# Performance work log

Measured on AMD Instinct MI355X. Metric: run time of the kernel, lower is better.

The kernel has to match this reference:

```python
import jax, jax.numpy as jnp
import numpy as np
import math

N = 100000
E = 1600000
IN_DIM = 64
OUT_DIM = 64
EPS = 1e-5


def setup_inputs() -> dict:
    key = jax.random.key(0)
    ks = jax.random.split(key, 12)
    s = 1.0 / math.sqrt(IN_DIM)
    inp = {
        "geo_x": jax.random.normal(ks[0], (N, IN_DIM), dtype=jnp.float32),
        "euc_x": jax.random.normal(ks[1], (N, IN_DIM), dtype=jnp.float32),
        "Wq": jax.random.uniform(ks[2], (OUT_DIM, IN_DIM), minval=-s, maxval=s, dtype=jnp.float32),
        "bq": jnp.zeros((OUT_DIM,), jnp.float32),
        "Wk": jax.random.uniform(ks[3], (OUT_DIM, IN_DIM), minval=-s, maxval=s, dtype=jnp.float32),
        "bk": jnp.zeros((OUT_DIM,), jnp.float32),
        "Wv": jax.random.uniform(ks[4], (OUT_DIM, IN_DIM), minval=-s, maxval=s, dtype=jnp.float32),
        "bv": jnp.zeros((OUT_DIM,), jnp.float32),
        "Wskip": jax.random.uniform(ks[5], (OUT_DIM, IN_DIM), minval=-s, maxval=s, dtype=jnp.float32),
        "bskip": jnp.zeros((OUT_DIM,), jnp.float32),
        "ln_w": jnp.ones((OUT_DIM,), jnp.float32),
        "ln_b": jnp.zeros((OUT_DIM,), jnp.float32),
        "edge_index": jax.random.randint(ks[6], (2, E), 0, N, dtype=jnp.int64),
    }
    return inp


def reference(geo_x, euc_x, Wq, bq, Wk, bk, Wv, bv, Wskip, bskip, ln_w, ln_b, edge_index):
    n = euc_x.shape[0]
    src, dst = edge_index[0], edge_index[1]

    # TransformerConv, heads=1: q from target (euc), k/v from source (geo)
    q = euc_x @ Wq.T + bq                      # [N, C]
    k = geo_x @ Wk.T + bk                      # [N, C]
    v = geo_x @ Wv.T + bv                      # [N, C]
    C = q.shape[-1]

    # per-edge attention logits
    alpha = jnp.sum(q[dst] * k[src], axis=-1) / math.sqrt(C)   # [E]

    # segment softmax over incoming edges of each destination node
    amax = jax.ops.segment_max(alpha, dst, num_segments=n)
    amax = jnp.where(jnp.isfinite(amax), amax, 0.0)
    ex = jnp.exp(alpha - amax[dst])
    denom = jax.ops.segment_sum(ex, dst, num_segments=n)
    w = ex / (denom[dst] + 1e-16)                              # [E]

    # scatter-aggregate weighted values + root (skip) transform
    agg = jax.ops.segment_sum(w[:, None] * v[src], dst, num_segments=n)  # [N, C]
    out = agg + euc_x @ Wskip.T + bskip

    # PyG LayerNorm, mode='graph', batch=None: normalize over all nodes+channels
    mean = out.mean()
    xc = out - mean
    std = jnp.sqrt(jnp.mean(xc * xc))
    out = xc / (std + EPS) * ln_w + ln_b

    return jax.nn.relu(out)
```

## Files before the change

kernel.cpp:

```cpp
#include <hip/hip_runtime.h>
#include <hip/hip_fp16.h>


using short8 = __attribute__((ext_vector_type(8))) short;
using f32x4  = __attribute__((ext_vector_type(4))) float;
using h2     = __attribute__((ext_vector_type(2))) _Float16;

#define QSCALE 31.75f
#define VDESC  0.031496062992f
#define SCI    1.7889250e-4f

#define CAP   4608
#define NCBMAX 400

__device__ inline unsigned short f2bf(float f) {
    unsigned u = __float_as_uint(f);
    unsigned r = u + 0x7FFFu + ((u >> 16) & 1u);
    return (unsigned short)(r >> 16);
}
__device__ inline unsigned short f2h(float f) {
    union { _Float16 h; unsigned short u; } c;
    c.h = (_Float16)f;
    return c.u;
}
__device__ inline h2 u2h2(unsigned u) {
    union { unsigned u; h2 h; } c; c.u = u; return c.h;
}
__device__ inline signed char f2i8(float f) {
    float v = f * QSCALE;
    v = fminf(fmaxf(v, -127.f), 127.f);
    return (signed char)__float2int_rn(v);
}

__device__ inline float fexp2(float x) {
#if __has_builtin(__builtin_amdgcn_exp2f)
    return __builtin_amdgcn_exp2f(x);
#else
    return __expf(x * 0.6931471805599453f);
#endif
}

__device__ inline int dot8i(uint2 q, uint2 k) {
#if __has_builtin(__builtin_amdgcn_sdot4)
    int t = __builtin_amdgcn_sdot4((int)q.x, (int)k.x, 0, false);
    return  __builtin_amdgcn_sdot4((int)q.y, (int)k.y, t, false);
#else
    int t = 0;
    #pragma unroll
    for (int i = 0; i < 4; ++i) {
        int qa = (int)(q.x << (24 - 8 * i)) >> 24;
        int ka = (int)(k.x << (24 - 8 * i)) >> 24;
        int qb = (int)(q.y << (24 - 8 * i)) >> 24;
        int kb = (int)(k.y << (24 - 8 * i)) >> 24;
        t += qa * ka + qb * kb;
    }
    return t;
#endif
}

__global__ __launch_bounds__(256) void k0_wconv(
    const float* __restrict__ Wq, const float* __restrict__ Wk,
    const float* __restrict__ Wv, const float* __restrict__ Wsk,
    unsigned short* __restrict__ wbf, int* __restrict__ zbase, int zcount)
{
    if (blockIdx.x == 16) {
        for (int i = threadIdx.x; i < zcount; i += 256) zbase[i] = 0;
        return;
    }
    int mat = blockIdx.x >> 2;
    int i4  = (blockIdx.x & 3) * 256 + threadIdx.x;
    const float* W = (mat == 0) ? Wq : (mat == 1) ? Wk : (mat == 2) ? Wv : Wsk;
    float4 w = *(const float4*)(W + (long)i4 * 4);
    ushort4 o;
    o.x = f2bf(w.x); o.y = f2bf(w.y); o.z = f2bf(w.z); o.w = f2bf(w.w);
    *(ushort4*)(wbf + (long)mat * 4096 + (long)i4 * 4) = o;
}

__global__ __launch_bounds__(256, 3) void k1_proj(
    const float* __restrict__ geo, const float* __restrict__ euc,
    const unsigned short* __restrict__ wbf,
    const float* __restrict__ bq, const float* __restrict__ bk,
    const float* __restrict__ bv, const float* __restrict__ bsk,
    signed char* __restrict__ q8b, signed char* __restrict__ kv8,
    unsigned short* __restrict__ skb, int N)
{
    __shared__ __align__(16) char smem[4 * 64 * 208];
    const int tid  = threadIdx.x;
    const int lane = tid & 63;
    const int w    = tid >> 6;
    const int qq   = lane >> 4;
    const int m    = lane & 15;
    const long base = (long)blockIdx.x * 128;

    char* te0 = smem;
    char* te1 = smem + 64 * 208;
    char* tg0 = smem + 2 * 64 * 208;
    char* tg1 = smem + 3 * 64 * 208;

    const long nodeA0 = base + w * 16 + m;
    const long nodeA1 = base + 64 + w * 16 + m;

    auto loadA = [&](const float* __restrict__ x, long node, short8 a[2]) {
        const float* px = x + node * 64;
        const bool v = (node < N);
        #pragma unroll
        for (int kh = 0; kh < 2; ++kh) {
            float4 f0 = v ? *(const float4*)(px + kh * 32 + qq * 8)
                          : make_float4(0.f, 0.f, 0.f, 0.f);
            float4 f1 = v ? *(const float4*)(px + kh * 32 + qq * 8 + 4)
                          : make_float4(0.f, 0.f, 0.f, 0.f);
            short8 r;
            r[0] = (short)f2bf(f0.x); r[1] = (short)f2bf(f0.y);
            r[2] = (short)f2bf(f0.z); r[3] = (short)f2bf(f0.w);
            r[4] = (short)f2bf(f1.x); r[5] = (short)f2bf(f1.y);
            r[6] = (short)f2bf(f1.z); r[7] = (short)f2bf(f1.w);
            a[kh] = r;
        }
    };
    auto loadB = [&](int mat, short8 b[2][4]) {
        #pragma unroll
        for (int kh = 0; kh < 2; ++kh)
            #pragma unroll
            for (int nt = 0; nt < 4; ++nt)
                b[kh][nt] = *(const short8*)(wbf + (long)mat * 4096 +
                                             (nt * 16 + m) * 64 + kh * 32 + qq * 8);
    };
    auto mmul = [&](const short8 a[2], const short8 b[2][4], f32x4 acc[4]) {
        #pragma unroll
        for (int nt = 0; nt < 4; ++nt) acc[nt] = (f32x4)(0.f);
        #pragma unroll
        for (int kh = 0; kh < 2; ++kh)
            #pragma unroll
            for (int nt = 0; nt < 4; ++nt)
                acc[nt] = __builtin_amdgcn_mfma_f32_16x16x32_bf16(a[kh], b[kh][nt], acc[nt], 0, 0, 0);
    };

    auto emit_i8 = [&](const f32x4 acc[4], const float* __restrict__ bias, char* tile) {
        #pragma unroll
        for (int nt = 0; nt < 4; ++nt) {
            int c = nt * 16 + m;
            float bs = bias[c];
            #pragma unroll
            for (int r = 0; r < 4; ++r) {
                int nl = w * 16 + qq * 4 + r;
                *(signed char*)(tile + nl * 208 + c) = f2i8(acc[nt][r] + bs);
            }
        }
    };
    auto emit_h = [&](const f32x4 acc[4], const float* __restrict__ bias, char* tile) {
        #pragma unroll
        for (int nt = 0; nt < 4; ++nt) {
            int c = nt * 16 + m;
            float bs = bias[c];
            #pragma unroll
            for (int r = 0; r < 4; ++r) {
                int nl = w * 16 + qq * 4 + r;
                *(unsigned short*)(tile + nl * 208 + 64 + c * 2) = f2h(acc[nt][r] + bs);
            }
        }
    };
    auto emit_kv = [&](const f32x4 acc[4], const float* __restrict__ bias,
                       char* tile, int vpart) {
        #pragma unroll
        for (int nt = 0; nt < 4; ++nt) {
            int c = nt * 16 + m;
            float bs = bias[c];
            int boff = (c >> 3) * 16 + vpart * 8 + (c & 7);
            #pragma unroll
            for (int r = 0; r < 4; ++r) {
                int nl = w * 16 + qq * 4 + r;
                *(signed char*)(tile + nl * 208 + boff) = f2i8(acc[nt][r] + bs);
            }
        }
    };

    short8 a0[2], a1[2];
    short8 B0[2][4], B1[2][4];
    f32x4 acc[4];

    loadA(euc, nodeA0, a0);
    loadA(euc, nodeA1, a1);
    loadB(0, B0);
    loadB(3, B1);
    mmul(a0, B0, acc); emit_i8(acc, bq, te0);
    mmul(a1, B0, acc); emit_i8(acc, bq, te1);
    mmul(a0, B1, acc); emit_h(acc, bsk, te0);
    mmul(a1, B1, acc); emit_h(acc, bsk, te1);

    loadA(geo, nodeA0, a0);
    loadA(geo, nodeA1, a1);
    loadB(1, B0);
    loadB(2, B1);
    mmul(a0, B0, acc); emit_kv(acc, bk, tg0, 0);
    mmul(a1, B0, acc); emit_kv(acc, bk, tg1, 0);
    mmul(a0, B1, acc); emit_kv(acc, bv, tg0, 1);
    mmul(a1, B1, acc); emit_kv(acc, bv, tg1, 1);
    __syncthreads();

    #pragma unroll
    for (int t = 0; t < 2; ++t) {
        const char* te = t ? te1 : te0;
        const char* tg = t ? tg1 : tg0;
        const long tb = base + t * 64;
        {
            int n = tid >> 2, j = tid & 3;
            long nd = tb + n;
            if (nd < N)
                *(int4*)(q8b + nd * 64 + j * 16) = *(const int4*)(te + n * 208 + j * 16);
        }
        #pragma unroll
        for (int it = 0; it < 2; ++it) {
            int idx = it * 256 + tid;
            int n = idx >> 3, j = idx & 7;
            long nd = tb + n;
            if (nd < N)
                *(int4*)((char*)skb + nd * 128 + j * 16) =
                    *(const int4*)(te + n * 208 + 64 + j * 16);
        }
        #pragma unroll
        for (int it = 0; it < 2; ++it) {
            int idx = it * 256 + tid;
            int n = idx >> 3, j = idx & 7;
            long nd = tb + n;
            if (nd < N)
                *(int4*)(kv8 + nd * 128 + j * 16) = *(const int4*)(tg + n * 208 + j * 16);
        }
    }
}

__global__ __launch_bounds__(512) void k2a_part(
    const int* __restrict__ ei, int E, int N,
    int* __restrict__ ccur, unsigned* __restrict__ tmp)
{
    __shared__ unsigned ebuf[4096];
    __shared__ unsigned short cbuf[4096];
    __shared__ int h[NCBMAX], offA[NCBMAX], lc[NCBMAX], creg[NCBMAX];
    __shared__ int sc[512];

    const int tid = threadIdx.x;
    const int NCB = (N + 255) >> 8;
    const long e0 = (long)blockIdx.x * 4096;
    const int tileN = (int)(((long)E - e0 < 4096) ? ((long)E - e0) : 4096);

    for (int i = tid; i < NCB; i += 512) { h[i] = 0; lc[i] = 0; }
    __syncthreads();

    const int* srcp = ei;
    const int* dstp = ei + E;
    unsigned wj[8];
    int cbj[8];
    #pragma unroll
    for (int j = 0; j < 8; ++j) {
        int i = j * 512 + tid;
        wj[j] = 0u; cbj[j] = -1;
        if (i < tileN) {
            int d = dstp[e0 + i], s = srcp[e0 + i];
            cbj[j] = d >> 8;
            wj[j]  = ((unsigned)(d & 255) << 17) | (unsigned)s;
            atomicAdd(&h[cbj[j]], 1);
        }
    }
    __syncthreads();

    sc[tid] = (tid < NCB) ? h[tid] : 0;
    __syncthreads();
    int own = sc[tid];
    for (int off = 1; off < 512; off <<= 1) {
        int v = (tid >= off) ? sc[tid - off] : 0;
        __syncthreads();
        sc[tid] += v;
        __syncthreads();
    }
    if (tid < NCB) offA[tid] = sc[tid] - own;
    if (tid < NCB && h[tid] > 0)
        creg[tid] = atomicAdd(&ccur[tid], h[tid]);
    __syncthreads();

    #pragma unroll
    for (int j = 0; j < 8; ++j) {
        if (cbj[j] >= 0) {
            int pos = offA[cbj[j]] + atomicAdd(&lc[cbj[j]], 1);
            ebuf[pos] = wj[j];
            cbuf[pos] = (unsigned short)cbj[j];
        }
    }
    __syncthreads();

    #pragma unroll
    for (int j = 0; j < 8; ++j) {
        int i = j * 512 + tid;
        if (i < tileN) {
            int cb = cbuf[i];
            int r  = creg[cb] + (i - offA[cb]);
            if (r < CAP) tmp[(long)cb * CAP + r] = ebuf[i];
        }
    }
}

__global__ __launch_bounds__(512, 8) void k3_attn(
    const signed char* __restrict__ q8b, const signed char* __restrict__ kv8,
    const unsigned short* __restrict__ skb,
    const int* __restrict__ ccnt, const unsigned* __restrict__ tmp,
    float* __restrict__ out, float* __restrict__ partS, float* __restrict__ partSS,
    int N)
{
    __shared__ unsigned bkt[64 * 65];
    __shared__ int dcnt[64];
    __shared__ unsigned char perm[64];
    __shared__ float redS[8], redSS[8];
    const int tid  = threadIdx.x;
    const int lane = tid & 63;
    const int w    = tid >> 6;
    const int g0   = tid >> 3;
    const int gl   = tid & 7;
    const int bin  = blockIdx.x;
    const int cb   = bin >> 2;
    const unsigned sub = (unsigned)(bin & 3);
    const long nodeBase = (long)bin * 64;

    if (tid < 64) dcnt[tid] = 0;
    __syncthreads();

    int len = ccnt[cb];
    if (len > CAP) len = CAP;
    const unsigned* reg = tmp + (long)cb * CAP;
    for (int e = tid; e < len; e += 512) {
        unsigned wv = reg[e];
        if (((wv >> 23) & 3u) == sub) {
            int d = (wv >> 17) & 63;
            int slot = atomicAdd(&dcnt[d], 1);
            if (slot < 64) bkt[d * 65 + slot] = wv & 0x1FFFFu;
        }
    }
    __syncthreads();

    if (tid < 64) {
        int d = dcnt[tid]; if (d > 64) d = 64;
        int r = 0;
        for (int j = 0; j < 64; ++j) {
            int dj = dcnt[j]; if (dj > 64) dj = 64;
            r += (dj > d) || ((dj == d) && (j < tid));
        }
        perm[r] = (unsigned char)tid;
    }
    __syncthreads();

    const int row  = perm[g0];
    const long node = nodeBase + row;

    uint2 qu = make_uint2(0, 0);
    if (node < N) qu = *(const uint2*)(q8b + node * 64 + gl * 8);

    int deg = dcnt[row];
    if (deg > 64) deg = 64;

    float den = 0.f;
    float a0=0.f,a1=0.f,a2=0.f,a3=0.f,a4=0.f,a5=0.f,a6=0.f,a7=0.f;

    auto vacc = [&](unsigned vx, unsigned vy, float ex) {
        a0 = fmaf((float)((int)(vx << 24) >> 24), ex, a0);
        a1 = fmaf((float)((int)(vx << 16) >> 24), ex, a1);
        a2 = fmaf((float)((int)(vx <<  8) >> 24), ex, a2);
        a3 = fmaf((float)((int)(vx      ) >> 24), ex, a3);
        a4 = fmaf((float)((int)(vy << 24) >> 24), ex, a4);
        a5 = fmaf((float)((int)(vy << 16) >> 24), ex, a5);
        a6 = fmaf((float)((int)(vy <<  8) >> 24), ex, a6);
        a7 = fmaf((float)((int)(vy      ) >> 24), ex, a7);
    };

    if (deg > 0) {
        const int rb  = row * 65;
        const int dm1 = deg - 1;
        unsigned sA = bkt[rb];
        uint4 rA = *(const uint4*)(kv8 + (long)sA * 128 + gl * 16);

        for (int s = 0; s < deg; s += 2) {
            int i1 = (s + 1 < deg) ? s + 1 : dm1;
            unsigned sB = bkt[rb + i1];
            uint4 rB = *(const uint4*)(kv8 + (long)sB * 128 + gl * 16);

            int t0 = dot8i(qu, make_uint2(rA.x, rA.y));
            t0 += __shfl_xor(t0, 1);
            t0 += __shfl_xor(t0, 2);
            t0 += __shfl_xor(t0, 4);
            float ex0 = fexp2((float)t0 * SCI);
            den += ex0;
            vacc(rA.z, rA.w, ex0);

            int i2 = (s + 2 < deg) ? s + 2 : dm1;
            unsigned sC = bkt[rb + i2];
            rA = *(const uint4*)(kv8 + (long)sC * 128 + gl * 16);

            int t1 = dot8i(qu, make_uint2(rB.x, rB.y));
            t1 += __shfl_xor(t1, 1);
            t1 += __shfl_xor(t1, 2);
            t1 += __shfl_xor(t1, 4);
            float ex1 = (s + 1 < deg) ? fexp2((float)t1 * SCI) : 0.f;
            den += ex1;
            vacc(rB.z, rB.w, ex1);
        }
    }

    float sacc = 0.f, ssacc = 0.f;
    if (node < N) {
        float inv = VDESC / (den + 1e-16f);
        uint4 sk = *(const uint4*)((const char*)skb + node * 128 + gl * 16);
        h2 s0 = u2h2(sk.x), s1 = u2h2(sk.y), s2 = u2h2(sk.z), s3 = u2h2(sk.w);
        float o0 = a0 * inv + (float)s0.x, o1 = a1 * inv + (float)s0.y;
        float o2 = a2 * inv + (float)s1.x, o3 = a3 * inv + (float)s1.y;
        float o4 = a4 * inv + (float)s2.x, o5 = a5 * inv + (float)s2.y;
        float o6 = a6 * inv + (float)s3.x, o7 = a7 * inv + (float)s3.y;
        *(float4*)(out + node * 64 + gl * 8)     = make_float4(o0, o1, o2, o3);
        *(float4*)(out + node * 64 + gl * 8 + 4) = make_float4(o4, o5, o6, o7);
        sacc  = (o0 + o1 + o2 + o3) + (o4 + o5 + o6 + o7);
        ssacc = o0*o0 + o1*o1 + o2*o2 + o3*o3 + o4*o4 + o5*o5 + o6*o6 + o7*o7;
    }
    #pragma unroll
    for (int m = 1; m <= 32; m <<= 1) {
        sacc  += __shfl_xor(sacc, m);
        ssacc += __shfl_xor(ssacc, m);
    }
    if (lane == 0) { redS[w] = sacc; redSS[w] = ssacc; }
    __syncthreads();
    if (tid == 0) {
        float s = 0.f, ss = 0.f;
        #pragma unroll
        for (int i = 0; i < 8; ++i) { s += redS[i]; ss += redSS[i]; }
        partS[bin]  = s;
        partSS[bin] = ss;
    }
}

__global__ __launch_bounds__(256) void k35_stats(
    const float* __restrict__ partS, const float* __restrict__ partSS,
    int nparts, float* __restrict__ stats, float M)
{
    __shared__ float rs[256], rss[256];
    float s = 0.f, ss = 0.f;
    for (int i = threadIdx.x; i < nparts; i += 256) { s += partS[i]; ss += partSS[i]; }
    rs[threadIdx.x] = s; rss[threadIdx.x] = ss;
    __syncthreads();
    for (int st = 128; st > 0; st >>= 1) {
        if (threadIdx.x < st) {
            rs[threadIdx.x]  += rs[threadIdx.x + st];
            rss[threadIdx.x] += rss[threadIdx.x + st];
        }
        __syncthreads();
    }
    if (threadIdx.x == 0) {
        float mean = rs[0] / M;
        float var  = rss[0] / M - mean * mean;
        if (var < 0.f) var = 0.f;
        stats[0] = mean;
        stats[1] = 1.f / (sqrtf(var) + 1e-5f);
    }
}

__global__ __launch_bounds__(256) void k4_ln(
    float* __restrict__ out, const float* __restrict__ lnw,
    const float* __restrict__ lnb, const float* __restrict__ stats, int M4)
{
    int i = blockIdx.x * 256 + threadIdx.x;
    if (i >= M4) return;
    float mean = stats[0], scale = stats[1];
    float4 x = *(float4*)(out + (long)i * 4);
    int c4 = (i & 15) * 4;
    float4 wv = *(const float4*)(lnw + c4);
    float4 bv = *(const float4*)(lnb + c4);
    x.x = fmaxf((x.x - mean) * scale * wv.x + bv.x, 0.f);
    x.y = fmaxf((x.y - mean) * scale * wv.y + bv.y, 0.f);
    x.z = fmaxf((x.z - mean) * scale * wv.z + bv.z, 0.f);
    x.w = fmaxf((x.w - mean) * scale * wv.w + bv.w, 0.f);
    *(float4*)(out + (long)i * 4) = x;
}

extern "C" void kernel_launch(void* const* d_in, const int* in_sizes, int n_in,
                              void* d_out, int out_size, void* d_ws, size_t ws_size,
                              hipStream_t stream)
{
    const float* geo = (const float*)d_in[0];
    const float* euc = (const float*)d_in[1];
    const float* Wq  = (const float*)d_in[2];
    const float* bq  = (const float*)d_in[3];
    const float* Wk  = (const float*)d_in[4];
    const float* bk  = (const float*)d_in[5];
    const float* Wv  = (const float*)d_in[6];
    const float* bv  = (const float*)d_in[7];
    const float* Wsk = (const float*)d_in[8];
    const float* bsk = (const float*)d_in[9];
    const float* lnw = (const float*)d_in[10];
    const float* lnb = (const float*)d_in[11];
    const int*   ei  = (const int*)d_in[12];

    const int N = in_sizes[0] / 64;
    const int E = in_sizes[12] / 2;
    const int K = (N + 63) / 64;
    const int NCB = (N + 255) >> 8;
    float* out = (float*)d_out;

    char* p = (char*)d_ws;
    signed char*    q8b   = (signed char*)p;    p += (size_t)N * 64;
    signed char*    kv8   = (signed char*)p;    p += (size_t)N * 128;
    unsigned short* skb   = (unsigned short*)p; p += (size_t)N * 64 * 2;
    unsigned*       tmp   = (unsigned*)p;       p += (size_t)NCB * CAP * 4;
    unsigned short* wbf   = (unsigned short*)p; p += (size_t)4 * 4096 * 2;
    int* ccur = (int*)p;  p += (size_t)(NCB + 8) * 4;
    float* partS  = (float*)p; p += (size_t)K * 4;
    float* partSS = (float*)p; p += (size_t)K * 4;
    float* stats  = (float*)p;

    const int PB2 = (N + 127) / 128;

    k0_wconv<<<17, 256, 0, stream>>>(Wq, Wk, Wv, Wsk, wbf, ccur, NCB + 8);
    k1_proj<<<PB2, 256, 0, stream>>>(geo, euc, wbf, bq, bk, bv, bsk,
                                     q8b, kv8, skb, N);
    const int GA = (E + 4095) / 4096;
    k2a_part<<<GA, 512, 0, stream>>>(ei, E, N, ccur, tmp);
    k3_attn<<<K, 512, 0, stream>>>(q8b, kv8, skb, ccur, tmp, out, partS, partSS, N);
    k35_stats<<<1, 256, 0, stream>>>(partS, partSS, K, stats, (float)N * 64.0f);
    const int M4 = N * 16;
    k4_ln<<<(M4 + 255) / 256, 256, 0, stream>>>(out, lnw, lnb, stats, M4);
}
```

Before: 212.1 us.

## Store pre-norm output as fp16, widen attention bins, add nontemporal memory ops

The attention kernel now handles 128 destination nodes per block, two per 8-lane group, and stores the pre-LayerNorm result as packed fp16 in a new workspace buffer rather than fp32 in the output. The LayerNorm kernel reads that fp16 buffer and writes fp32 with nontemporal stores, cutting intermediate traffic. The projection kernel halves its shared memory by running the euc and geo phases one after the other, and its occupancy hint rises to 6. Streaming loads and stores across kernels use nontemporal builtins. The fp16 intermediate loses some precision, and the serialized projection phases add a barrier.

```diff
diff --git a/kernel.cpp b/kernel.cpp
--- a/kernel.cpp
+++ b/kernel.cpp
@@ -5,6 +5,9 @@
 using short8 = __attribute__((ext_vector_type(8))) short;
 using f32x4  = __attribute__((ext_vector_type(4))) float;
 using h2     = __attribute__((ext_vector_type(2))) _Float16;
+using u32x4  = __attribute__((ext_vector_type(4))) unsigned;
+using u32x2  = __attribute__((ext_vector_type(2))) unsigned;
+using f32x4v = __attribute__((ext_vector_type(4))) float;
 
 #define QSCALE 31.75f
 #define VDESC  0.031496062992f
@@ -12,6 +15,36 @@
 
 #define CAP   4608
 #define NCBMAX 400
+
+__device__ inline int ntload(const int* p) {
+    return __builtin_nontemporal_load(p);
+}
+__device__ inline unsigned ntload(const unsigned* p) {
+    return __builtin_nontemporal_load(p);
+}
+__device__ inline uint2 ntload(const uint2* p) {
+    u32x2 v = __builtin_nontemporal_load((const u32x2*)p);
+    return make_uint2(v.x, v.y);
+}
+__device__ inline uint4 ntload(const uint4* p) {
+    u32x4 v = __builtin_nontemporal_load((const u32x4*)p);
+    return make_uint4(v.x, v.y, v.z, v.w);
+}
+__device__ inline float4 ntload(const float4* p) {
+    f32x4v v = __builtin_nontemporal_load((const f32x4v*)p);
+    return make_float4(v.x, v.y, v.z, v.w);
+}
+__device__ inline void ntstore(unsigned* p, unsigned v) {
+    __builtin_nontemporal_store(v, p);
+}
+__device__ inline void ntstore(uint4* p, uint4 v) {
+    u32x4 t; t.x = v.x; t.y = v.y; t.z = v.z; t.w = v.w;
+    __builtin_nontemporal_store(t, (u32x4*)p);
+}
+__device__ inline void ntstore(float4* p, float4 v) {
+    f32x4v t; t.x = v.x; t.y = v.y; t.z = v.z; t.w = v.w;
+    __builtin_nontemporal_store(t, (f32x4v*)p);
+}
 
 __device__ inline unsigned short f2bf(float f) {
     unsigned u = __float_as_uint(f);
@@ -76,7 +109,7 @@
     *(ushort4*)(wbf + (long)mat * 4096 + (long)i4 * 4) = o;
 }
 
-__global__ __launch_bounds__(256, 3) void k1_proj(
+__global__ __launch_bounds__(256, 6) void k1_proj(
     const float* __restrict__ geo, const float* __restrict__ euc,
     const unsigned short* __restrict__ wbf,
     const float* __restrict__ bq, const float* __restrict__ bk,
@@ -84,7 +117,7 @@
     signed char* __restrict__ q8b, signed char* __restrict__ kv8,
     unsigned short* __restrict__ skb, int N)
 {
-    __shared__ __align__(16) char smem[4 * 64 * 208];
+    __shared__ __align__(16) char smem[2 * 64 * 208];
     const int tid  = threadIdx.x;
     const int lane = tid & 63;
     const int w    = tid >> 6;
@@ -92,10 +125,8 @@
     const int m    = lane & 15;
     const long base = (long)blockIdx.x * 128;
 
-    char* te0 = smem;
-    char* te1 = smem + 64 * 208;
-    char* tg0 = smem + 2 * 64 * 208;
-    char* tg1 = smem + 3 * 64 * 208;
+    char* t0 = smem;
+    char* t1 = smem + 64 * 208;
 
     const long nodeA0 = base + w * 16 + m;
     const long nodeA1 = base + 64 + w * 16 + m;
@@ -105,9 +136,9 @@
         const bool v = (node < N);
         #pragma unroll
         for (int kh = 0; kh < 2; ++kh) {
-            float4 f0 = v ? *(const float4*)(px + kh * 32 + qq * 8)
+            float4 f0 = v ? ntload((const float4*)(px + kh * 32 + qq * 8))
                           : make_float4(0.f, 0.f, 0.f, 0.f);
-            float4 f1 = v ? *(const float4*)(px + kh * 32 + qq * 8 + 4)
+            float4 f1 = v ? ntload((const float4*)(px + kh * 32 + qq * 8 + 4))
                           : make_float4(0.f, 0.f, 0.f, 0.f);
             short8 r;
             r[0] = (short)f2bf(f0.x); r[1] = (short)f2bf(f0.y);
@@ -182,25 +213,14 @@
     loadA(euc, nodeA1, a1);
     loadB(0, B0);
     loadB(3, B1);
-    mmul(a0, B0, acc); emit_i8(acc, bq, te0);
-    mmul(a1, B0, acc); emit_i8(acc, bq, te1);
-    mmul(a0, B1, acc); emit_h(acc, bsk, te0);
-    mmul(a1, B1, acc); emit_h(acc, bsk, te1);
-
-    loadA(geo, nodeA0, a0);
-    loadA(geo, nodeA1, a1);
-    loadB(1, B0);
-    loadB(2, B1);
-    mmul(a0, B0, acc); emit_kv(acc, bk, tg0, 0);
-    mmul(a1, B0, acc); emit_kv(acc, bk, tg1, 0);
-    mmul(a0, B1, acc); emit_kv(acc, bv, tg0, 1);
-    mmul(a1, B1, acc); emit_kv(acc, bv, tg1, 1);
-    __syncthreads();
-
+    mmul(a0, B0, acc); emit_i8(acc, bq, t0);
+    mmul(a1, B0, acc); emit_i8(acc, bq, t1);
+    mmul(a0, B1, acc); emit_h(acc, bsk, t0);
+    mmul(a1, B1, acc); emit_h(acc, bsk, t1);
+    __syncthreads();
     #pragma unroll
     for (int t = 0; t < 2; ++t) {
-        const char* te = t ? te1 : te0;
-        const char* tg = t ? tg1 : tg0;
+        const char* te = t ? t1 : t0;
         const long tb = base + t * 64;
         {
             int n = tid >> 2, j = tid & 3;
@@ -217,6 +237,22 @@
                 *(int4*)((char*)skb + nd * 128 + j * 16) =
                     *(const int4*)(te + n * 208 + 64 + j * 16);
         }
+    }
+    __syncthreads();
+
+    loadA(geo, nodeA0, a0);
+    loadA(geo, nodeA1, a1);
+    loadB(1, B0);
+    loadB(2, B1);
+    mmul(a0, B0, acc); emit_kv(acc, bk, t0, 0);
+    mmul(a1, B0, acc); emit_kv(acc, bk, t1, 0);
+    mmul(a0, B1, acc); emit_kv(acc, bv, t0, 1);
+    mmul(a1, B1, acc); emit_kv(acc, bv, t1, 1);
+    __syncthreads();
+    #pragma unroll
+    for (int t = 0; t < 2; ++t) {
+        const char* tg = t ? t1 : t0;
+        const long tb = base + t * 64;
         #pragma unroll
         for (int it = 0; it < 2; ++it) {
             int idx = it * 256 + tid;
@@ -254,7 +290,7 @@
         int i = j * 512 + tid;
         wj[j] = 0u; cbj[j] = -1;
         if (i < tileN) {
-            int d = dstp[e0 + i], s = srcp[e0 + i];
+            int d = ntload(&dstp[e0 + i]), s = ntload(&srcp[e0 + i]);
             cbj[j] = d >> 8;
             wj[j]  = ((unsigned)(d & 255) << 17) | (unsigned)s;
             atomicAdd(&h[cbj[j]], 1);
@@ -292,7 +328,7 @@
         if (i < tileN) {
             int cb = cbuf[i];
             int r  = creg[cb] + (i - offA[cb]);
-            if (r < CAP) tmp[(long)cb * CAP + r] = ebuf[i];
+            if (r < CAP) ntstore(&tmp[(long)cb * CAP + r], ebuf[i]);
         }
     }
 }
@@ -301,12 +337,12 @@
     const signed char* __restrict__ q8b, const signed char* __restrict__ kv8,
     const unsigned short* __restrict__ skb,
     const int* __restrict__ ccnt, const unsigned* __restrict__ tmp,
-    float* __restrict__ out, float* __restrict__ partS, float* __restrict__ partSS,
-    int N)
-{
-    __shared__ unsigned bkt[64 * 65];
-    __shared__ int dcnt[64];
-    __shared__ unsigned char perm[64];
+    unsigned short* __restrict__ preb,
+    float* __restrict__ partS, float* __restrict__ partSS, int N)
+{
+    __shared__ unsigned bkt[128 * 65];
+    __shared__ int dcnt[128];
+    __shared__ unsigned char perm[128];
     __shared__ float redS[8], redSS[8];
     const int tid  = threadIdx.x;
     const int lane = tid & 63;
@@ -314,30 +350,30 @@
     const int g0   = tid >> 3;
     const int gl   = tid & 7;
     const int bin  = blockIdx.x;
-    const int cb   = bin >> 2;
-    const unsigned sub = (unsigned)(bin & 3);
-    const long nodeBase = (long)bin * 64;
-
-    if (tid < 64) dcnt[tid] = 0;
+    const int cb   = bin >> 1;
+    const unsigned sub = (unsigned)(bin & 1);
+    const long nodeBase = (long)bin * 128;
+
+    if (tid < 128) dcnt[tid] = 0;
     __syncthreads();
 
     int len = ccnt[cb];
     if (len > CAP) len = CAP;
     const unsigned* reg = tmp + (long)cb * CAP;
     for (int e = tid; e < len; e += 512) {
-        unsigned wv = reg[e];
-        if (((wv >> 23) & 3u) == sub) {
-            int d = (wv >> 17) & 63;
+        unsigned wv = ntload(&reg[e]);
+        if (((wv >> 24) & 1u) == sub) {
+            int d = (wv >> 17) & 127;
             int slot = atomicAdd(&dcnt[d], 1);
             if (slot < 64) bkt[d * 65 + slot] = wv & 0x1FFFFu;
         }
     }
     __syncthreads();
 
-    if (tid < 64) {
+    if (tid < 128) {
         int d = dcnt[tid]; if (d > 64) d = 64;
         int r = 0;
-        for (int j = 0; j < 64; ++j) {
+        for (int j = 0; j < 128; ++j) {
             int dj = dcnt[j]; if (dj > 64) dj = 64;
             r += (dj > d) || ((dj == d) && (j < tid));
         }
@@ -345,76 +381,84 @@
     }
     __syncthreads();
 
-    const int row  = perm[g0];
-    const long node = nodeBase + row;
-
-    uint2 qu = make_uint2(0, 0);
-    if (node < N) qu = *(const uint2*)(q8b + node * 64 + gl * 8);
-
-    int deg = dcnt[row];
-    if (deg > 64) deg = 64;
-
-    float den = 0.f;
-    float a0=0.f,a1=0.f,a2=0.f,a3=0.f,a4=0.f,a5=0.f,a6=0.f,a7=0.f;
-
-    auto vacc = [&](unsigned vx, unsigned vy, float ex) {
-        a0 = fmaf((float)((int)(vx << 24) >> 24), ex, a0);
-        a1 = fmaf((float)((int)(vx << 16) >> 24), ex, a1);
-        a2 = fmaf((float)((int)(vx <<  8) >> 24), ex, a2);
-        a3 = fmaf((float)((int)(vx      ) >> 24), ex, a3);
-        a4 = fmaf((float)((int)(vy << 24) >> 24), ex, a4);
-        a5 = fmaf((float)((int)(vy << 16) >> 24), ex, a5);
-        a6 = fmaf((float)((int)(vy <<  8) >> 24), ex, a6);
-        a7 = fmaf((float)((int)(vy      ) >> 24), ex, a7);
-    };
-
-    if (deg > 0) {
-        const int rb  = row * 65;
-        const int dm1 = deg - 1;
-        unsigned sA = bkt[rb];
-        uint4 rA = *(const uint4*)(kv8 + (long)sA * 128 + gl * 16);
-
-        for (int s = 0; s < deg; s += 2) {
-            int i1 = (s + 1 < deg) ? s + 1 : dm1;
-            unsigned sB = bkt[rb + i1];
-            uint4 rB = *(const uint4*)(kv8 + (long)sB * 128 + gl * 16);
-
-            int t0 = dot8i(qu, make_uint2(rA.x, rA.y));
-            t0 += __shfl_xor(t0, 1);
-            t0 += __shfl_xor(t0, 2);
-            t0 += __shfl_xor(t0, 4);
-            float ex0 = fexp2((float)t0 * SCI);
-            den += ex0;
-            vacc(rA.z, rA.w, ex0);
-
-            int i2 = (s + 2 < deg) ? s + 2 : dm1;
-            unsigned sC = bkt[rb + i2];
-            rA = *(const uint4*)(kv8 + (long)sC * 128 + gl * 16);
-
-            int t1 = dot8i(qu, make_uint2(rB.x, rB.y));
-            t1 += __shfl_xor(t1, 1);
-            t1 += __shfl_xor(t1, 2);
-            t1 += __shfl_xor(t1, 4);
-            float ex1 = (s + 1 < deg) ? fexp2((float)t1 * SCI) : 0.f;
-            den += ex1;
-            vacc(rB.z, rB.w, ex1);
-        }
-    }
-
     float sacc = 0.f, ssacc = 0.f;
-    if (node < N) {
-        float inv = VDESC / (den + 1e-16f);
-        uint4 sk = *(const uint4*)((const char*)skb + node * 128 + gl * 16);
-        h2 s0 = u2h2(sk.x), s1 = u2h2(sk.y), s2 = u2h2(sk.z), s3 = u2h2(sk.w);
-        float o0 = a0 * inv + (float)s0.x, o1 = a1 * inv + (float)s0.y;
-        float o2 = a2 * inv + (float)s1.x, o3 = a3 * inv + (float)s1.y;
-        float o4 = a4 * inv + (float)s2.x, o5 = a5 * inv + (float)s2.y;
-        float o6 = a6 * inv + (float)s3.x, o7 = a7 * inv + (float)s3.y;
-        *(float4*)(out + node * 64 + gl * 8)     = make_float4(o0, o1, o2, o3);
-        *(float4*)(out + node * 64 + gl * 8 + 4) = make_float4(o4, o5, o6, o7);
-        sacc  = (o0 + o1 + o2 + o3) + (o4 + o5 + o6 + o7);
-        ssacc = o0*o0 + o1*o1 + o2*o2 + o3*o3 + o4*o4 + o5*o5 + o6*o6 + o7*o7;
-    }
+
+    for (int half = 0; half < 2; ++half) {
+        const int row  = perm[half ? (127 - g0) : g0];
+        const long node = nodeBase + row;
+
+        uint2 qu = make_uint2(0, 0);
+        if (node < N) qu = ntload((const uint2*)(q8b + node * 64 + gl * 8));
+
+        int deg = dcnt[row];
+        if (deg > 64) deg = 64;
+
+        float den = 0.f;
+        float a0=0.f,a1=0.f,a2=0.f,a3=0.f,a4=0.f,a5=0.f,a6=0.f,a7=0.f;
+
+        auto vacc = [&](unsigned vx, unsigned vy, float ex) {
+            a0 = fmaf((float)((int)(vx << 24) >> 24), ex, a0);
+            a1 = fmaf((float)((int)(vx << 16) >> 24), ex, a1);
+            a2 = fmaf((float)((int)(vx <<  8) >> 24), ex, a2);
+            a3 = fmaf((float)((int)(vx      ) >> 24), ex, a3);
+            a4 = fmaf((float)((int)(vy << 24) >> 24), ex, a4);
+            a5 = fmaf((float)((int)(vy << 16) >> 24), ex, a5);
+            a6 = fmaf((float)((int)(vy <<  8) >> 24), ex, a6);
+            a7 = fmaf((float)((int)(vy      ) >> 24), ex, a7);
+        };
+
+        if (deg > 0) {
+            const int rb  = row * 65;
+            const int dm1 = deg - 1;
+            unsigned sA = bkt[rb];
+            uint4 rA = *(const uint4*)(kv8 + (long)sA * 128 + gl * 16);
+
+            for (int s = 0; s < deg; s += 2) {
+                int i1 = (s + 1 < deg) ? s + 1 : dm1;
+                unsigned sB = bkt[rb + i1];
+                uint4 rB = *(const uint4*)(kv8 + (long)sB * 128 + gl * 16);
+
+                int t0 = dot8i(qu, make_uint2(rA.x, rA.y));
+                t0 += __shfl_xor(t0, 1);
+                t0 += __shfl_xor(t0, 2);
+                t0 += __shfl_xor(t0, 4);
+                float ex0 = fexp2((float)t0 * SCI);
+                den += ex0;
+                vacc(rA.z, rA.w, ex0);
+
+                int i2 = (s + 2 < deg) ? s + 2 : dm1;
+                unsigned sC = bkt[rb + i2];
+                rA = *(const uint4*)(kv8 + (long)sC * 128 + gl * 16);
+
+                int t1 = dot8i(qu, make_uint2(rB.x, rB.y));
+                t1 += __shfl_xor(t1, 1);
+                t1 += __shfl_xor(t1, 2);
+                t1 += __shfl_xor(t1, 4);
+                float ex1 = (s + 1 < deg) ? fexp2((float)t1 * SCI) : 0.f;
+                den += ex1;
+                vacc(rB.z, rB.w, ex1);
+            }
+        }
+
+        if (node < N) {
+            float inv = VDESC / (den + 1e-16f);
+            uint4 sk = ntload((const uint4*)((const char*)skb + node * 128 + gl * 16));
+            h2 s0 = u2h2(sk.x), s1 = u2h2(sk.y), s2 = u2h2(sk.z), s3 = u2h2(sk.w);
+            float o0 = a0 * inv + (float)s0.x, o1 = a1 * inv + (float)s0.y;
+            float o2 = a2 * inv + (float)s1.x, o3 = a3 * inv + (float)s1.y;
+            float o4 = a4 * inv + (float)s2.x, o5 = a5 * inv + (float)s2.y;
+            float o6 = a6 * inv + (float)s3.x, o7 = a7 * inv + (float)s3.y;
+            uint4 ov;
+            ov.x = (unsigned)f2h(o0) | ((unsigned)f2h(o1) << 16);
+            ov.y = (unsigned)f2h(o2) | ((unsigned)f2h(o3) << 16);
+            ov.z = (unsigned)f2h(o4) | ((unsigned)f2h(o5) << 16);
+            ov.w = (unsigned)f2h(o6) | ((unsigned)f2h(o7) << 16);
+            ntstore((uint4*)((char*)preb + node * 128 + gl * 16), ov);
+            sacc  += (o0 + o1 + o2 + o3) + (o4 + o5 + o6 + o7);
+            ssacc += o0*o0 + o1*o1 + o2*o2 + o3*o3 + o4*o4 + o5*o5 + o6*o6 + o7*o7;
+        }
+    }
+
     #pragma unroll
     for (int m = 1; m <= 32; m <<= 1) {
         sacc  += __shfl_xor(sacc, m);
@@ -457,21 +501,31 @@
 }
 
 __global__ __launch_bounds__(256) void k4_ln(
-    float* __restrict__ out, const float* __restrict__ lnw,
-    const float* __restrict__ lnb, const float* __restrict__ stats, int M4)
+    const unsigned short* __restrict__ preb, float* __restrict__ out,
+    const float* __restrict__ lnw, const float* __restrict__ lnb,
+    const float* __restrict__ stats, int M8)
 {
     int i = blockIdx.x * 256 + threadIdx.x;
-    if (i >= M4) return;
+    if (i >= M8) return;
     float mean = stats[0], scale = stats[1];
-    float4 x = *(float4*)(out + (long)i * 4);
-    int c4 = (i & 15) * 4;
-    float4 wv = *(const float4*)(lnw + c4);
-    float4 bv = *(const float4*)(lnb + c4);
-    x.x = fmaxf((x.x - mean) * scale * wv.x + bv.x, 0.f);
-    x.y = fmaxf((x.y - mean) * scale * wv.y + bv.y, 0.f);
-    x.z = fmaxf((x.z - mean) * scale * wv.z + bv.z, 0.f);
-    x.w = fmaxf((x.w - mean) * scale * wv.w + bv.w, 0.f);
-    *(float4*)(out + (long)i * 4) = x;
+    uint4 pv = ntload((const uint4*)((const char*)preb + (size_t)i * 16));
+    int c8 = (i & 7) * 8;
+    float4 w0 = *(const float4*)(lnw + c8);
+    float4 w1 = *(const float4*)(lnw + c8 + 4);
+    float4 b0 = *(const float4*)(lnb + c8);
+    float4 b1 = *(const float4*)(lnb + c8 + 4);
+    h2 p0 = u2h2(pv.x), p1 = u2h2(pv.y), p2 = u2h2(pv.z), p3 = u2h2(pv.w);
+    float4 r0, r1;
+    r0.x = fmaxf(((float)p0.x - mean) * scale * w0.x + b0.x, 0.f);
+    r0.y = fmaxf(((float)p0.y - mean) * scale * w0.y + b0.y, 0.f);
+    r0.z = fmaxf(((float)p1.x - mean) * scale * w0.z + b0.z, 0.f);
+    r0.w = fmaxf(((float)p1.y - mean) * scale * w0.w + b0.w, 0.f);
+    r1.x = fmaxf(((float)p2.x - mean) * scale * w1.x + b1.x, 0.f);
+    r1.y = fmaxf(((float)p2.y - mean) * scale * w1.y + b1.y, 0.f);
+    r1.z = fmaxf(((float)p3.x - mean) * scale * w1.z + b1.z, 0.f);
+    r1.w = fmaxf(((float)p3.y - mean) * scale * w1.w + b1.w, 0.f);
+    ntstore((float4*)(out + (size_t)i * 8), r0);
+    ntstore((float4*)(out + (size_t)i * 8 + 4), r1);
 }
 
 extern "C" void kernel_launch(void* const* d_in, const int* in_sizes, int n_in,
@@ -494,7 +548,7 @@
 
     const int N = in_sizes[0] / 64;
     const int E = in_sizes[12] / 2;
-    const int K = (N + 63) / 64;
+    const int KB = (N + 127) / 128;
     const int NCB = (N + 255) >> 8;
     float* out = (float*)d_out;
 
@@ -502,11 +556,12 @@
     signed char*    q8b   = (signed char*)p;    p += (size_t)N * 64;
     signed char*    kv8   = (signed char*)p;    p += (size_t)N * 128;
     unsigned short* skb   = (unsigned short*)p; p += (size_t)N * 64 * 2;
+    unsigned short* preb  = (unsigned short*)p; p += (size_t)N * 64 * 2;
     unsigned*       tmp   = (unsigned*)p;       p += (size_t)NCB * CAP * 4;
     unsigned short* wbf   = (unsigned short*)p; p += (size_t)4 * 4096 * 2;
     int* ccur = (int*)p;  p += (size_t)(NCB + 8) * 4;
-    float* partS  = (float*)p; p += (size_t)K * 4;
-    float* partSS = (float*)p; p += (size_t)K * 4;
+    float* partS  = (float*)p; p += (size_t)KB * 4;
+    float* partSS = (float*)p; p += (size_t)KB * 4;
     float* stats  = (float*)p;
 
     const int PB2 = (N + 127) / 128;
@@ -516,8 +571,9 @@
                                      q8b, kv8, skb, N);
     const int GA = (E + 4095) / 4096;
     k2a_part<<<GA, 512, 0, stream>>>(ei, E, N, ccur, tmp);
-    k3_attn<<<K, 512, 0, stream>>>(q8b, kv8, skb, ccur, tmp, out, partS, partSS, N);
-    k35_stats<<<1, 256, 0, stream>>>(partS, partSS, K, stats, (float)N * 64.0f);
-    const int M4 = N * 16;
-    k4_ln<<<(M4 + 255) / 256, 256, 0, stream>>>(out, lnw, lnb, stats, M4);
-}
+    k3_attn<<<KB, 512, 0, stream>>>(q8b, kv8, skb, ccur, tmp, preb,
+                                    partS, partSS, N);
+    k35_stats<<<1, 256, 0, stream>>>(partS, partSS, KB, stats, (float)N * 64.0f);
+    const int M8 = N * 8;
+    k4_ln<<<(M8 + 255) / 256, 256, 0, stream>>>(preb, out, lnw, lnb, stats, M8);
+}
```

After: 244.4 us. 15.3% more time.
